# Kernel optimization log

Measured on AMD Instinct MI355X. Metric: run time of the kernel, lower is better.

The kernel has to match this reference:

```python
import jax, jax.numpy as jnp
import numpy as np

TAU = 1.0
NUM_CLASSES = 14
LOSS_WEIGHT = 1.0
KSUM = 27.0  # sum of the 3x3x3 all-ones kernel


def setup_inputs() -> dict:
    key = jax.random.key(0)
    k1, k2, k3 = jax.random.split(key, 3)
    shape = (2, 14, 96, 96, 96)
    return {
        "preds_S": jax.random.normal(k1, shape, dtype=jnp.float32),
        "preds_T": jax.random.normal(k2, shape, dtype=jnp.float32),
        "outputs_T": jax.random.normal(k3, shape, dtype=jnp.float32),
    }


def _boundaries(targets):
    # targets: [B, H, W, D] int class map. For each class, boundary voxels are
    # those where the 3x3x3 box-sum of the one-hot mask is in (0, 27):
    # conv==27 (fully interior) is zeroed, conv>0 is set to 1.
    onehot = jax.nn.one_hot(targets, NUM_CLASSES, axis=1, dtype=jnp.float32)  # [B,K,H,W,D]
    box = jax.lax.reduce_window(
        onehot, 0.0, jax.lax.add,
        window_dimensions=(1, 1, 3, 3, 3),
        window_strides=(1, 1, 1, 1, 1),
        padding=((0, 0), (0, 0), (1, 1), (1, 1), (1, 1)),
    )
    return jnp.where((box > 0) & (box != KSUM), 1.0, 0.0)  # [B,K,H,W,D]


def reference(preds_S, preds_T, outputs_T):
    B, C = preds_S.shape[:2]
    targets = jnp.argmax(outputs_T, axis=1)  # [B,H,W,D] (detached in original)
    boundary = _boundaries(targets).reshape(B, NUM_CLASSES, -1)  # [B,K,V]

    sS = preds_S.reshape(B, C, -1) / TAU
    sT = preds_T.reshape(B, C, -1) / TAU
    log_s = jax.nn.log_softmax(sS, axis=1)   # softmax over class dim (dim=0 of [C,V] view)
    log_t = jax.nn.log_softmax(sT, axis=1)
    t = jnp.exp(log_t)
    # pointwise KL summed over classes per voxel: [B,V]
    pk = jnp.sum(t * (log_t - log_s), axis=1)

    n = jnp.sum(boundary, axis=-1)                      # [B,K] boundary voxel counts
    num = jnp.einsum('bkv,bv->bk', boundary, pk)        # KL mass on boundary voxels
    # KLDivLoss(reduction='mean') divides by numel = C * n; skip empty boundaries
    term = jnp.where(n > 0, num / (C * jnp.maximum(n, 1.0)), 0.0)
    return LOSS_WEIGHT * (TAU ** 2) * jnp.sum(term)
```

## Files before the change

kernel.cpp:

```cpp
#include <hip/hip_runtime.h>

#define NC 14
#define DIM 96
#define NV (DIM*DIM*DIM)
#define NV4 (NV/4)
#define WS2 112
#define HS2 (112*98)
#define PADV (112*98*98)
#define SLABB ((size_t)PADV*2*2)

typedef float f4 __attribute__((ext_vector_type(4)));

__global__ void __launch_bounds__(256)
argmax_bit_kernel(const float* __restrict__ outT, unsigned short* __restrict__ bm) {
    int tid = blockIdx.x * 256 + threadIdx.x;
    int b = tid >= NV4;
    int q = tid - b * NV4;
    int v4 = q * 4;
    const float* po = outT + (size_t)b * NC * NV + v4;
    f4 best = *(const f4*)po;
    int b0 = 0, b1 = 0, b2 = 0, b3 = 0;
#pragma unroll
    for (int c = 1; c < NC; ++c) {
        f4 v = *(const f4*)(po + (size_t)c * NV);
        if (v.x > best.x) { best.x = v.x; b0 = c; }
        if (v.y > best.y) { best.y = v.y; b1 = c; }
        if (v.z > best.z) { best.z = v.z; b2 = c; }
        if (v.w > best.w) { best.w = v.w; b3 = c; }
    }
    int d = v4 % DIM;
    int t1 = v4 / DIM;
    int w = t1 % DIM;
    int h = t1 / DIM;
    ushort4 bits;
    bits.x = (unsigned short)(1u << b0);
    bits.y = (unsigned short)(1u << b1);
    bits.z = (unsigned short)(1u << b2);
    bits.w = (unsigned short)(1u << b3);
    *(ushort4*)(bm + (size_t)b * PADV + (h + 1) * HS2 + (w + 1) * WS2 + (d + 8)) = bits;
}

__global__ void __launch_bounds__(256)
or_d_kernel(const unsigned short* __restrict__ bm, unsigned short* __restrict__ dm,
            float* __restrict__ acc) {
    if (blockIdx.x == 0 && threadIdx.x < 64) acc[threadIdx.x * 16] = 0.f;
    int idx = blockIdx.x * 256 + threadIdx.x;
    if (idx >= 2 * PADV / 8) return;
    int base = idx * 8;
    int pd0 = base % WS2;
    if (pd0 < 8 || pd0 > 96) return;
    uint4 X = *(const uint4*)(bm + base);
    unsigned x[10];
    x[0] = (pd0 == 8)  ? 0u : (unsigned)bm[base - 1];
    x[9] = (pd0 == 96) ? 0u : (unsigned)bm[base + 8];
    x[1] = X.x & 0xFFFFu; x[2] = X.x >> 16;
    x[3] = X.y & 0xFFFFu; x[4] = X.y >> 16;
    x[5] = X.z & 0xFFFFu; x[6] = X.z >> 16;
    x[7] = X.w & 0xFFFFu; x[8] = X.w >> 16;
    unsigned r[8];
#pragma unroll
    for (int j = 0; j < 8; ++j) r[j] = x[j] | x[j + 1] | x[j + 2];
    uint4 out;
    out.x = r[0] | (r[1] << 16);
    out.y = r[2] | (r[3] << 16);
    out.z = r[4] | (r[5] << 16);
    out.w = r[6] | (r[7] << 16);
    *(uint4*)(dm + base) = out;
}

__global__ void __launch_bounds__(256)
or_w_kernel(const unsigned short* __restrict__ dm, unsigned short* __restrict__ wm) {
    int idx = blockIdx.x * 256 + threadIdx.x;
    if (idx >= 2 * PADV / 8) return;
    int base = idx * 8;
    int pd0 = base % WS2;
    if (pd0 < 8 || pd0 > 96) return;
    int pw = ((base % PADV) / WS2) % 98;
    if (pw < 1 || pw > 96) return;
    uint4 c = *(const uint4*)(dm + base);
    uint4 a = {0u, 0u, 0u, 0u}, e = {0u, 0u, 0u, 0u};
    if (pw > 1)  a = *(const uint4*)(dm + base - WS2);
    if (pw < 96) e = *(const uint4*)(dm + base + WS2);
    uint4 out;
    out.x = a.x | c.x | e.x;
    out.y = a.y | c.y | e.y;
    out.z = a.z | c.z | e.z;
    out.w = a.w | c.w | e.w;
    *(uint4*)(wm + base) = out;
}

__global__ void __launch_bounds__(256)
boundary_kl_kernel(const float* __restrict__ pS, const float* __restrict__ pT,
                   const unsigned short* __restrict__ wm,
                   float* __restrict__ acc) {
    const int b = blockIdx.x & 1;
    int tid4 = (blockIdx.x >> 1) * 256 + threadIdx.x;
    int v4 = tid4 * 4;
    int d = v4 % DIM;
    int t1 = v4 / DIM;
    int w = t1 % DIM;
    int h = t1 / DIM;

    const float* sS = pS + (size_t)b * NC * NV + v4;
    const float* sT = pT + (size_t)b * NC * NV + v4;
    const unsigned short* w0 = wm + (size_t)b * PADV;

    int off = (h + 1) * HS2 + (w + 1) * WS2 + (d + 8);
    ushort4 m1 = *(const ushort4*)(w0 + off);
    ushort4 m0 = {0, 0, 0, 0}, m2 = {0, 0, 0, 0};
    if (h > 0)  m0 = *(const ushort4*)(w0 + off - HS2);
    if (h < 95) m2 = *(const ushort4*)(w0 + off + HS2);

    f4 seS = {0, 0, 0, 0}, seT = {0, 0, 0, 0}, dot = {0, 0, 0, 0};
#pragma unroll
    for (int c = 0; c < NC; ++c) {
        f4 vs = __builtin_nontemporal_load((const f4*)(sS + (size_t)c * NV));
        f4 vt = __builtin_nontemporal_load((const f4*)(sT + (size_t)c * NV));
        float e;
        seS.x += __expf(vs.x); e = __expf(vt.x); seT.x += e; dot.x += e * (vt.x - vs.x);
        seS.y += __expf(vs.y); e = __expf(vt.y); seT.y += e; dot.y += e * (vt.y - vs.y);
        seS.z += __expf(vs.z); e = __expf(vt.z); seT.z += e; dot.z += e * (vt.z - vs.z);
        seS.w += __expf(vs.w); e = __expf(vt.w); seT.w += e; dot.w += e * (vt.w - vs.w);
    }
    float pk[4];
    pk[0] = dot.x / seT.x + __logf(seS.x) - __logf(seT.x);
    pk[1] = dot.y / seT.y + __logf(seS.y) - __logf(seT.y);
    pk[2] = dot.z / seT.z + __logf(seS.z) - __logf(seT.z);
    pk[3] = dot.w / seT.w + __logf(seS.w) - __logf(seT.w);

    unsigned mk[4];
    mk[0] = (unsigned)(m0.x | m1.x | m2.x);
    mk[1] = (unsigned)(m0.y | m1.y | m2.y);
    mk[2] = (unsigned)(m0.z | m1.z | m2.z);
    mk[3] = (unsigned)(m0.w | m1.w | m2.w);

    bool hwint = ((unsigned)(h - 1) <= 93u) && ((unsigned)(w - 1) <= 93u);
    float num[NC], cnt[NC];
#pragma unroll
    for (int c = 0; c < NC; ++c) { num[c] = 0.f; cnt[c] = 0.f; }
#pragma unroll
    for (int j = 0; j < 4; ++j) {
        unsigned m = mk[j];
        if (hwint && ((unsigned)(d + j - 1) <= 93u) && (m & (m - 1)) == 0u) m = 0u;
        float p = pk[j];
#pragma unroll
        for (int c = 0; c < NC; ++c) {
            float hit = (float)((m >> c) & 1u);
            num[c] = fmaf(hit, p, num[c]);
            cnt[c] += hit;
        }
    }

    __shared__ float snum[NC], scnt[NC];
    if (threadIdx.x < NC) { snum[threadIdx.x] = 0.f; scnt[threadIdx.x] = 0.f; }
    __syncthreads();
    int lane = threadIdx.x & 63;
#pragma unroll
    for (int c = 0; c < NC; ++c) {
        float s = num[c], n = cnt[c];
#pragma unroll
        for (int o = 32; o; o >>= 1) {
            s += __shfl_xor(s, o);
            n += __shfl_xor(n, o);
        }
        if (lane == 0) {
            atomicAdd(&snum[c], s);
            atomicAdd(&scnt[c], n);
        }
    }
    __syncthreads();
    if (threadIdx.x < NC) {
        atomicAdd(&acc[(b * NC + threadIdx.x) * 16], snum[threadIdx.x]);
        atomicAdd(&acc[(32 + b * NC + threadIdx.x) * 16], scnt[threadIdx.x]);
    }
}

__global__ void finalize_kernel(const float* __restrict__ acc, float* __restrict__ out) {
    if (threadIdx.x == 0 && blockIdx.x == 0) {
        float s = 0.f;
        for (int i = 0; i < 2 * NC; ++i) {
            float n = acc[(32 + i) * 16];
            if (n > 0.f) s += acc[i * 16] / ((float)NC * n);
        }
        out[0] = s;
    }
}

extern "C" void kernel_launch(void* const* d_in, const int* in_sizes, int n_in,
                              void* d_out, int out_size, void* d_ws, size_t ws_size,
                              hipStream_t stream) {
    const float* preds_S = (const float*)d_in[0];
    const float* preds_T = (const float*)d_in[1];
    const float* outputs_T = (const float*)d_in[2];

    char* ws = (char*)d_ws;
    float* acc = (float*)ws;
    unsigned short* bm = (unsigned short*)(ws + 4096);
    unsigned short* dm = (unsigned short*)(ws + 4096 + SLABB);
    unsigned short* wm = bm;

    argmax_bit_kernel<<<(2 * NV4) / 256, 256, 0, stream>>>(outputs_T, bm);
    {
        int chunks = 2 * PADV / 8;
        int blocks = (chunks + 255) / 256;
        or_d_kernel<<<blocks, 256, 0, stream>>>(bm, dm, acc);
        or_w_kernel<<<blocks, 256, 0, stream>>>(dm, wm);
    }
    boundary_kl_kernel<<<2 * (NV4 / 256), 256, 0, stream>>>(preds_S, preds_T, wm, acc);
    finalize_kernel<<<1, 64, 0, stream>>>(acc, (float*)d_out);
}
```

Baseline: 82.12 us.

## Fuse d and w OR-dilation passes into one LDS-tiled in-place kernel

Replaces the two separate OR-dilation kernels along d and w with a single kernel. Each block loads one padded h-slice of the class bitmask into shared memory, does the 3x3 OR in w and d there, and writes the result back in place. This removes one launch and the global round-trip of the intermediate mask, but uses only 192 blocks with a ~22KB LDS tile each, so occupancy during this stage is low. It also adds a launch_bounds occupancy hint of 8 on the main KL kernel.

```diff
diff --git a/kernel.cpp b/kernel.cpp
--- a/kernel.cpp
+++ b/kernel.cpp
@@ -41,55 +41,59 @@
 }
 
 __global__ void __launch_bounds__(256)
-or_d_kernel(const unsigned short* __restrict__ bm, unsigned short* __restrict__ dm,
-            float* __restrict__ acc) {
+or_dw_kernel(unsigned short* __restrict__ mask, float* __restrict__ acc) {
     if (blockIdx.x == 0 && threadIdx.x < 64) acc[threadIdx.x * 16] = 0.f;
-    int idx = blockIdx.x * 256 + threadIdx.x;
-    if (idx >= 2 * PADV / 8) return;
-    int base = idx * 8;
-    int pd0 = base % WS2;
-    if (pd0 < 8 || pd0 > 96) return;
-    uint4 X = *(const uint4*)(bm + base);
-    unsigned x[10];
-    x[0] = (pd0 == 8)  ? 0u : (unsigned)bm[base - 1];
-    x[9] = (pd0 == 96) ? 0u : (unsigned)bm[base + 8];
-    x[1] = X.x & 0xFFFFu; x[2] = X.x >> 16;
-    x[3] = X.y & 0xFFFFu; x[4] = X.y >> 16;
-    x[5] = X.z & 0xFFFFu; x[6] = X.z >> 16;
-    x[7] = X.w & 0xFFFFu; x[8] = X.w >> 16;
-    unsigned r[8];
-#pragma unroll
-    for (int j = 0; j < 8; ++j) r[j] = x[j] | x[j + 1] | x[j + 2];
-    uint4 out;
-    out.x = r[0] | (r[1] << 16);
-    out.y = r[2] | (r[3] << 16);
-    out.z = r[4] | (r[5] << 16);
-    out.w = r[6] | (r[7] << 16);
-    *(uint4*)(dm + base) = out;
-}
-
-__global__ void __launch_bounds__(256)
-or_w_kernel(const unsigned short* __restrict__ dm, unsigned short* __restrict__ wm) {
-    int idx = blockIdx.x * 256 + threadIdx.x;
-    if (idx >= 2 * PADV / 8) return;
-    int base = idx * 8;
-    int pd0 = base % WS2;
-    if (pd0 < 8 || pd0 > 96) return;
-    int pw = ((base % PADV) / WS2) % 98;
-    if (pw < 1 || pw > 96) return;
-    uint4 c = *(const uint4*)(dm + base);
-    uint4 a = {0u, 0u, 0u, 0u}, e = {0u, 0u, 0u, 0u};
-    if (pw > 1)  a = *(const uint4*)(dm + base - WS2);
-    if (pw < 96) e = *(const uint4*)(dm + base + WS2);
-    uint4 out;
-    out.x = a.x | c.x | e.x;
-    out.y = a.y | c.y | e.y;
-    out.z = a.z | c.z | e.z;
-    out.w = a.w | c.w | e.w;
-    *(uint4*)(wm + base) = out;
-}
-
-__global__ void __launch_bounds__(256)
+
+    const int b = blockIdx.x & 1;
+    const int ph = (blockIdx.x >> 1) + 1;
+    unsigned short* slice = mask + (size_t)b * PADV + ph * HS2;
+
+    __shared__ unsigned short tile[98][WS2];
+    for (int i = threadIdx.x; i < 98 * WS2 / 2; i += 256)
+        ((unsigned*)tile)[i] = 0u;
+    __syncthreads();
+    for (int i = threadIdx.x; i < 96 * 12; i += 256) {
+        int row = 1 + i / 12;
+        int pd0 = 8 + (i % 12) * 8;
+        *(uint4*)&tile[row][pd0] = *(const uint4*)(slice + row * WS2 + pd0);
+    }
+    __syncthreads();
+
+    for (int i = threadIdx.x; i < 96 * 12; i += 256) {
+        int pw = 1 + i / 12;
+        int pd0 = 8 + (i % 12) * 8;
+        uint4 A = *(const uint4*)&tile[pw - 1][pd0];
+        uint4 B = *(const uint4*)&tile[pw][pd0];
+        uint4 C = *(const uint4*)&tile[pw + 1][pd0];
+        unsigned lft = (unsigned)tile[pw - 1][pd0 - 1] | (unsigned)tile[pw][pd0 - 1] |
+                       (unsigned)tile[pw + 1][pd0 - 1];
+        unsigned rgt = (unsigned)tile[pw - 1][pd0 + 8] | (unsigned)tile[pw][pd0 + 8] |
+                       (unsigned)tile[pw + 1][pd0 + 8];
+        uint4 W;
+        W.x = A.x | B.x | C.x;
+        W.y = A.y | B.y | C.y;
+        W.z = A.z | B.z | C.z;
+        W.w = A.w | B.w | C.w;
+        unsigned x[10];
+        x[0] = lft;
+        x[1] = W.x & 0xFFFFu; x[2] = W.x >> 16;
+        x[3] = W.y & 0xFFFFu; x[4] = W.y >> 16;
+        x[5] = W.z & 0xFFFFu; x[6] = W.z >> 16;
+        x[7] = W.w & 0xFFFFu; x[8] = W.w >> 16;
+        x[9] = rgt;
+        unsigned r[8];
+#pragma unroll
+        for (int j = 0; j < 8; ++j) r[j] = x[j] | x[j + 1] | x[j + 2];
+        uint4 out;
+        out.x = r[0] | (r[1] << 16);
+        out.y = r[2] | (r[3] << 16);
+        out.z = r[4] | (r[5] << 16);
+        out.w = r[6] | (r[7] << 16);
+        *(uint4*)(slice + pw * WS2 + pd0) = out;
+    }
+}
+
+__global__ void __launch_bounds__(256, 8)
 boundary_kl_kernel(const float* __restrict__ pS, const float* __restrict__ pT,
                    const unsigned short* __restrict__ wm,
                    float* __restrict__ acc) {
@@ -195,17 +199,10 @@
 
     char* ws = (char*)d_ws;
     float* acc = (float*)ws;
-    unsigned short* bm = (unsigned short*)(ws + 4096);
-    unsigned short* dm = (unsigned short*)(ws + 4096 + SLABB);
-    unsigned short* wm = bm;
-
-    argmax_bit_kernel<<<(2 * NV4) / 256, 256, 0, stream>>>(outputs_T, bm);
-    {
-        int chunks = 2 * PADV / 8;
-        int blocks = (chunks + 255) / 256;
-        or_d_kernel<<<blocks, 256, 0, stream>>>(bm, dm, acc);
-        or_w_kernel<<<blocks, 256, 0, stream>>>(dm, wm);
-    }
-    boundary_kl_kernel<<<2 * (NV4 / 256), 256, 0, stream>>>(preds_S, preds_T, wm, acc);
+    unsigned short* mask = (unsigned short*)(ws + 4096);
+
+    argmax_bit_kernel<<<(2 * NV4) / 256, 256, 0, stream>>>(outputs_T, mask);
+    or_dw_kernel<<<192, 256, 0, stream>>>(mask, acc);
+    boundary_kl_kernel<<<2 * (NV4 / 256), 256, 0, stream>>>(preds_S, preds_T, mask, acc);
     finalize_kernel<<<1, 64, 0, stream>>>(acc, (float*)d_out);
 }
```

Result: slower. 185.6 us (+126.0%).
